# Performance work log

Hardware: AMD Instinct MI355X
Metric: run time of the kernel (lower is better)

Reference implementation:

```python
import jax, jax.numpy as jnp
import numpy as np

EMB, HID, NH = 512, 256, 8
DH = HID // NH
LN_EPS = 1e-5


def _mk(key, shape, scale=0.02):
    return jax.random.normal(key, shape, dtype=jnp.float32) * scale


def setup_inputs() -> dict:
    key = jax.random.key(0)
    ks = jax.random.split(key, 24)
    B, S = 8, 256
    return {
        "memory_embeddings": jax.random.normal(ks[0], (B, S, EMB), dtype=jnp.float32),
        # memory_encoder: Linear(512,256) -> LayerNorm -> ReLU -> Linear(256,256)
        "enc_w1": _mk(ks[1], (HID, EMB)), "enc_b1": jnp.zeros((HID,), jnp.float32),
        "ln_g": jnp.ones((HID,), jnp.float32), "ln_b": jnp.zeros((HID,), jnp.float32),
        "enc_w2": _mk(ks[2], (HID, HID)), "enc_b2": jnp.zeros((HID,), jnp.float32),
        # MultiheadAttention packed qkv + out proj
        "in_proj_w": _mk(ks[3], (3 * HID, HID)), "in_proj_b": jnp.zeros((3 * HID,), jnp.float32),
        "out_w": _mk(ks[4], (HID, HID)), "out_b": jnp.zeros((HID,), jnp.float32),
        # consistency head: Linear(256,128) -> ReLU -> Linear(128,1) -> Sigmoid
        "cons_w1": _mk(ks[5], (HID // 2, HID)), "cons_b1": jnp.zeros((HID // 2,), jnp.float32),
        "cons_w2": _mk(ks[6], (1, HID // 2)), "cons_b2": jnp.zeros((1,), jnp.float32),
        # hallucination detector
        "hall_w1": _mk(ks[7], (HID // 2, HID)), "hall_b1": jnp.zeros((HID // 2,), jnp.float32),
        "hall_w2": _mk(ks[8], (1, HID // 2)), "hall_b2": jnp.zeros((1,), jnp.float32),
        # contradiction analyzer: Linear(512,256) -> ReLU -> Linear(256,1) -> Sigmoid
        "con_w1": _mk(ks[9], (HID, 2 * HID)), "con_b1": jnp.zeros((HID,), jnp.float32),
        "con_w2": _mk(ks[10], (1, HID)), "con_b2": jnp.zeros((1,), jnp.float32),
    }


def _forward(memory_embeddings, enc_w1, enc_b1, ln_g, ln_b, enc_w2, enc_b2,
             in_proj_w, in_proj_b, out_w, out_b,
             cons_w1, cons_b1, cons_w2, cons_b2,
             hall_w1, hall_b1, hall_w2, hall_b2,
             con_w1, con_b1, con_w2, con_b2):
    B, S, _ = memory_embeddings.shape
    # --- memory encoder (dropout in eval mode = identity) ---
    h = memory_embeddings @ enc_w1.T + enc_b1                      # [B,S,HID]
    mu = h.mean(-1, keepdims=True)
    var = ((h - mu) ** 2).mean(-1, keepdims=True)
    h = (h - mu) * jax.lax.rsqrt(var + LN_EPS) * ln_g + ln_b
    mf = jax.nn.relu(h) @ enc_w2.T + enc_b2                        # [B,S,HID]
    # --- multihead self-attention (batch_first, averaged attn weights) ---
    qkv = mf @ in_proj_w.T + in_proj_b                              # [B,S,3H]
    q, k, v = jnp.split(qkv, 3, axis=-1)
    def heads(t):  # [B,S,H] -> [B,NH,S,DH]
        return t.reshape(B, S, NH, DH).transpose(0, 2, 1, 3)
    q, k, v = heads(q), heads(k), heads(v)
    scores = jnp.einsum('bhsd,bhtd->bhst', q, k) / jnp.sqrt(jnp.float32(DH))
    attn = jax.nn.softmax(scores, axis=-1)                          # [B,NH,S,S]
    ctx = jnp.einsum('bhst,bhtd->bhsd', attn, v)
    ctx = ctx.transpose(0, 2, 1, 3).reshape(B, S, HID)
    attended = ctx @ out_w.T + out_b                                # [B,S,HID]
    attn_weights = attn.mean(axis=1)                                # [B,S,S]
    # --- pooled heads ---
    pooled = attended.mean(axis=1)                                  # [B,HID]
    cons = jax.nn.sigmoid(jax.nn.relu(pooled @ cons_w1.T + cons_b1) @ cons_w2.T + cons_b2)[:, 0]
    hall = jax.nn.sigmoid(jax.nn.relu(pooled @ hall_w1.T + hall_b1) @ hall_w2.T + hall_b2)[:, 0]
    # --- contradiction matrix over all i<j pairs (vectorized gather/MLP/scatter) ---
    iu, ju = np.triu_indices(S, k=1)                                # static indices
    Wa, Wb = con_w1[:, :HID], con_w1[:, HID:]                       # split concat-linear
    a = mf @ Wa.T                                                   # [B,S,HID]
    b = mf @ Wb.T
    hid = jax.nn.relu(a[:, iu] + b[:, ju] + con_b1)                 # [B,P,HID]
    sc = jax.nn.sigmoid(hid @ con_w2.T + con_b2)[..., 0]            # [B,P]
    M = jnp.zeros((B, S, S), dtype=mf.dtype)
    M = M.at[:, iu, ju].set(sc)
    M = M.at[:, ju, iu].set(sc)
    return cons, hall, M, attn_weights


def reference(memory_embeddings, enc_w1, enc_b1, ln_g, ln_b, enc_w2, enc_b2,
              in_proj_w, in_proj_b, out_w, out_b,
              cons_w1, cons_b1, cons_w2, cons_b2,
              hall_w1, hall_b1, hall_w2, hall_b2,
              con_w1, con_b1, con_w2, con_b2):
    return _forward(memory_embeddings, enc_w1, enc_b1, ln_g, ln_b, enc_w2, enc_b2,
                    in_proj_w, in_proj_b, out_w, out_b,
                    cons_w1, cons_b1, cons_w2, cons_b2,
                    hall_w1, hall_b1, hall_w2, hall_b2,
                    con_w1, con_b1, con_w2, con_b2)
```

## Files before the change

### kernel.cpp

```cpp
#include <hip/hip_runtime.h>
#include <math.h>

typedef __attribute__((ext_vector_type(8))) short bf16x8;
typedef __attribute__((ext_vector_type(4))) float f32x4;

__device__ __forceinline__ short f2b(float f) {
  union { float f; unsigned u; } v; v.f = f;
  unsigned u = v.u + 0x7fffu + ((v.u >> 16) & 1u);
  return (short)(u >> 16);
}

__global__ __launch_bounds__(256) void k_cvt(
    const float* __restrict__ w1, const float* __restrict__ w2,
    const float* __restrict__ wq, const float* __restrict__ wc,
    unsigned short* __restrict__ o, float* __restrict__ poolctx) {
  if (blockIdx.x == 0) {
    float4 z = {0.f, 0.f, 0.f, 0.f};
    ((float4*)poolctx)[threadIdx.x] = z;
    ((float4*)poolctx)[threadIdx.x + 256] = z;
  }
  int base = (blockIdx.x * 256 + threadIdx.x) * 4;
#pragma unroll
  for (int u = 0; u < 4; ++u) {
    int idx = base + u;
    float v;
    if (idx < 131072) v = w1[idx];
    else if (idx < 196608) v = w2[idx - 131072];
    else if (idx < 393216) v = wq[idx - 196608];
    else {
      int i = idx - 393216, n = i >> 8, k = i & 255;
      v = (n < 256) ? wc[n * 512 + k] : wc[(n - 256) * 512 + 256 + k];
    }
    o[idx] = (unsigned short)f2b(v);
  }
}

__global__ __launch_bounds__(256) void k_enc(
    const float* __restrict__ me,
    const unsigned short* __restrict__ wb1, const float* __restrict__ b1,
    const float* __restrict__ g, const float* __restrict__ lb,
    const unsigned short* __restrict__ wb2, const float* __restrict__ b2,
    unsigned short* __restrict__ mfb) {
  __shared__ float hh[16 * 260];
  __shared__ unsigned short rA[16 * 264];
  __shared__ unsigned short mfs[16 * 256];
  int tid = threadIdx.x, lane = tid & 63, w = tid >> 6;
  int row0 = blockIdx.x * 16;
  int m = lane & 15, q = lane >> 4;

  {
    f32x4 acc[4];
#pragma unroll
    for (int i = 0; i < 4; ++i) acc[i] = (f32x4){0.f, 0.f, 0.f, 0.f};
    const float* ap = me + (size_t)(row0 + m) * 512 + q * 8;
    float4 pa0[4], pa1[4];
    bf16x8 pb[4][4];
#pragma unroll
    for (int d = 0; d < 4; ++d) {
      pa0[d] = *(const float4*)(ap + d * 32);
      pa1[d] = *(const float4*)(ap + d * 32 + 4);
#pragma unroll
      for (int nt = 0; nt < 4; ++nt)
        pb[d][nt] = *(const bf16x8*)(wb1 + (size_t)(w * 64 + nt * 16 + m) * 512 + d * 32 + q * 8);
    }
#pragma unroll
    for (int it = 0; it < 16; ++it) {
      int slot = it & 3;
      float4 a01 = pa0[slot], a23 = pa1[slot];
      bf16x8 bl0 = pb[slot][0], bl1 = pb[slot][1];
      bf16x8 bl2 = pb[slot][2], bl3 = pb[slot][3];
      if (it + 4 < 16) {
        pa0[slot] = *(const float4*)(ap + (it + 4) * 32);
        pa1[slot] = *(const float4*)(ap + (it + 4) * 32 + 4);
#pragma unroll
        for (int nt = 0; nt < 4; ++nt)
          pb[slot][nt] = *(const bf16x8*)(wb1 + (size_t)(w * 64 + nt * 16 + m) * 512 + (it + 4) * 32 + q * 8);
      }
      bf16x8 af;
      af[0] = f2b(a01.x); af[1] = f2b(a01.y); af[2] = f2b(a01.z); af[3] = f2b(a01.w);
      af[4] = f2b(a23.x); af[5] = f2b(a23.y); af[6] = f2b(a23.z); af[7] = f2b(a23.w);
      acc[0] = __builtin_amdgcn_mfma_f32_16x16x32_bf16(af, bl0, acc[0], 0, 0, 0);
      acc[1] = __builtin_amdgcn_mfma_f32_16x16x32_bf16(af, bl1, acc[1], 0, 0, 0);
      acc[2] = __builtin_amdgcn_mfma_f32_16x16x32_bf16(af, bl2, acc[2], 0, 0, 0);
      acc[3] = __builtin_amdgcn_mfma_f32_16x16x32_bf16(af, bl3, acc[3], 0, 0, 0);
    }
#pragma unroll
    for (int nt = 0; nt < 4; ++nt) {
      int col = w * 64 + nt * 16 + m;
      float bias = b1[col];
#pragma unroll
      for (int reg = 0; reg < 4; ++reg)
        hh[(q * 4 + reg) * 260 + col] = acc[nt][reg] + bias;
    }
  }
  __syncthreads();
  {
    float4 g4 = *(const float4*)(g + lane * 4);
    float4 lb4 = *(const float4*)(lb + lane * 4);
#pragma unroll
    for (int rr = 0; rr < 4; ++rr) {
      int r = w * 4 + rr;
      float4 v = *(const float4*)&hh[r * 260 + lane * 4];
      float s1 = v.x + v.y + v.z + v.w;
      float s2 = v.x * v.x + v.y * v.y + v.z * v.z + v.w * v.w;
#pragma unroll
      for (int o = 32; o > 0; o >>= 1) {
        s1 += __shfl_xor(s1, o, 64);
        s2 += __shfl_xor(s2, o, 64);
      }
      float mu = s1 * (1.f / 256.f);
      float var = s2 * (1.f / 256.f) - mu * mu;
      float rs = rsqrtf(var + 1e-5f);
      unsigned short y0 = (unsigned short)f2b(fmaxf((v.x - mu) * rs * g4.x + lb4.x, 0.f));
      unsigned short y1 = (unsigned short)f2b(fmaxf((v.y - mu) * rs * g4.y + lb4.y, 0.f));
      unsigned short y2 = (unsigned short)f2b(fmaxf((v.z - mu) * rs * g4.z + lb4.z, 0.f));
      unsigned short y3 = (unsigned short)f2b(fmaxf((v.w - mu) * rs * g4.w + lb4.w, 0.f));
      uint2 pk;
      pk.x = (unsigned)y0 | ((unsigned)y1 << 16);
      pk.y = (unsigned)y2 | ((unsigned)y3 << 16);
      *(uint2*)&rA[r * 264 + lane * 4] = pk;
    }
  }
  __syncthreads();
  {
    f32x4 acc[4];
#pragma unroll
    for (int i = 0; i < 4; ++i) acc[i] = (f32x4){0.f, 0.f, 0.f, 0.f};
    bf16x8 pb[4][4];
#pragma unroll
    for (int d = 0; d < 4; ++d)
#pragma unroll
      for (int nt = 0; nt < 4; ++nt)
        pb[d][nt] = *(const bf16x8*)(wb2 + (size_t)(w * 64 + nt * 16 + m) * 256 + d * 32 + q * 8);
#pragma unroll
    for (int it = 0; it < 8; ++it) {
      int slot = it & 3;
      bf16x8 bl0 = pb[slot][0], bl1 = pb[slot][1];
      bf16x8 bl2 = pb[slot][2], bl3 = pb[slot][3];
      if (it + 4 < 8) {
#pragma unroll
        for (int nt = 0; nt < 4; ++nt)
          pb[slot][nt] = *(const bf16x8*)(wb2 + (size_t)(w * 64 + nt * 16 + m) * 256 + (it + 4) * 32 + q * 8);
      }
      bf16x8 af = *(const bf16x8*)&rA[m * 264 + it * 32 + q * 8];
      acc[0] = __builtin_amdgcn_mfma_f32_16x16x32_bf16(af, bl0, acc[0], 0, 0, 0);
      acc[1] = __builtin_amdgcn_mfma_f32_16x16x32_bf16(af, bl1, acc[1], 0, 0, 0);
      acc[2] = __builtin_amdgcn_mfma_f32_16x16x32_bf16(af, bl2, acc[2], 0, 0, 0);
      acc[3] = __builtin_amdgcn_mfma_f32_16x16x32_bf16(af, bl3, acc[3], 0, 0, 0);
    }
#pragma unroll
    for (int nt = 0; nt < 4; ++nt) {
      int col = w * 64 + nt * 16 + m;
      float bias = b2[col];
#pragma unroll
      for (int reg = 0; reg < 4; ++reg)
        mfs[(q * 4 + reg) * 256 + col] = (unsigned short)f2b(acc[nt][reg] + bias);
    }
  }
  __syncthreads();
  {
    const uint4* src = (const uint4*)mfs;
    uint4* dst = (uint4*)(mfb + (size_t)row0 * 256);
    dst[tid] = src[tid];
    dst[tid + 256] = src[tid + 256];
  }
}

__global__ __launch_bounds__(256) void k_proj5(
    const unsigned short* __restrict__ mfb,
    const unsigned short* __restrict__ wqk,
    const unsigned short* __restrict__ wab,
    const float* __restrict__ bq, const float* __restrict__ cb1,
    float* __restrict__ qkv, float* __restrict__ amat,
    float* __restrict__ bmat) {
  int tid = threadIdx.x, lane = tid & 63, w = tid >> 6;
  int row0 = blockIdx.x * 16;
  int part = blockIdx.y;
  int m = lane & 15, q = lane >> 4;
  const unsigned short* W = (part < 3) ? (wqk + (size_t)part * 65536)
                                       : (wab + (size_t)(part - 3) * 65536);
  bf16x8 a[8];
#pragma unroll
  for (int ks = 0; ks < 8; ++ks)
    a[ks] = *(const bf16x8*)(mfb + (size_t)(row0 + m) * 256 + ks * 32 + q * 8);
  f32x4 acc[4];
#pragma unroll
  for (int i = 0; i < 4; ++i) acc[i] = (f32x4){0.f, 0.f, 0.f, 0.f};
  bf16x8 pb[4][4];
#pragma unroll
  for (int d = 0; d < 4; ++d)
#pragma unroll
    for (int nt = 0; nt < 4; ++nt)
      pb[d][nt] = *(const bf16x8*)(W + (size_t)(w * 64 + nt * 16 + m) * 256 + d * 32 + q * 8);
#pragma unroll
  for (int it = 0; it < 8; ++it) {
    int slot = it & 3;
    bf16x8 bl0 = pb[slot][0], bl1 = pb[slot][1];
    bf16x8 bl2 = pb[slot][2], bl3 = pb[slot][3];
    if (it + 4 < 8) {
#pragma unroll
      for (int nt = 0; nt < 4; ++nt)
        pb[slot][nt] = *(const bf16x8*)(W + (size_t)(w * 64 + nt * 16 + m) * 256 + (it + 4) * 32 + q * 8);
    }
    acc[0] = __builtin_amdgcn_mfma_f32_16x16x32_bf16(a[it], bl0, acc[0], 0, 0, 0);
    acc[1] = __builtin_amdgcn_mfma_f32_16x16x32_bf16(a[it], bl1, acc[1], 0, 0, 0);
    acc[2] = __builtin_amdgcn_mfma_f32_16x16x32_bf16(a[it], bl2, acc[2], 0, 0, 0);
    acc[3] = __builtin_amdgcn_mfma_f32_16x16x32_bf16(a[it], bl3, acc[3], 0, 0, 0);
  }
#pragma unroll
  for (int nt = 0; nt < 4; ++nt) {
    int col = w * 64 + nt * 16 + m;
    float bias;
    float* dst;
    int ld;
    if (part < 3) { bias = bq[part * 256 + col]; dst = qkv + part * 256; ld = 768; }
    else if (part == 3) { bias = cb1[col]; dst = amat; ld = 256; }
    else { bias = 0.f; dst = bmat; ld = 256; }
#pragma unroll
    for (int reg = 0; reg < 4; ++reg) {
      int row = row0 + q * 4 + reg;
      dst[(size_t)row * ld + col] = acc[nt][reg] + bias;
    }
  }
}

__global__ __launch_bounds__(256) void k_attn_fused(
    const float* __restrict__ qkv, unsigned short* __restrict__ attnb,
    float* __restrict__ poolctx) {
  __shared__ float qs[32 * 32];
  __shared__ unsigned short ps[32 * 264];
  __shared__ unsigned short vt[32 * 264];
  int blk = blockIdx.x;
  int sg = blk & 7, bh = blk >> 3, h = bh & 7, b = bh >> 3;
  int tid = threadIdx.x, lane = tid & 63, w = tid >> 6;
  {
    int r = tid >> 3, c4 = tid & 7;
    float4 v = *(const float4*)(qkv + ((size_t)(b * 256 + sg * 32 + r)) * 768 + h * 32 + c4 * 4);
    *(float4*)&qs[r * 32 + c4 * 4] = v;
  }
  {
    const float4* vr = (const float4*)(qkv + ((size_t)(b * 256 + tid)) * 768 + 512 + h * 32);
#pragma unroll
    for (int d4 = 0; d4 < 8; ++d4) {
      float4 vv = vr[d4];
      vt[(d4 * 4 + 0) * 264 + tid] = (unsigned short)f2b(vv.x);
      vt[(d4 * 4 + 1) * 264 + tid] = (unsigned short)f2b(vv.y);
      vt[(d4 * 4 + 2) * 264 + tid] = (unsigned short)f2b(vv.z);
      vt[(d4 * 4 + 3) * 264 + tid] = (unsigned short)f2b(vv.w);
    }
  }
  __syncthreads();
  int r0 = w * 8;
  float sc[8][4];
#pragma unroll
  for (int r = 0; r < 8; ++r)
#pragma unroll
    for (int tt = 0; tt < 4; ++tt) sc[r][tt] = 0.f;
#pragma unroll
  for (int tt = 0; tt < 4; ++tt) {
    int t = tt * 64 + lane;
    const float4* kp = (const float4*)(qkv + ((size_t)(b * 256 + t)) * 768 + 256 + h * 32);
#pragma unroll
    for (int d4 = 0; d4 < 8; ++d4) {
      float4 kv = kp[d4];
#pragma unroll
      for (int r = 0; r < 8; ++r) {
        float4 qv = *(const float4*)&qs[(r0 + r) * 32 + d4 * 4];
        sc[r][tt] += qv.x * kv.x + qv.y * kv.y + qv.z * kv.z + qv.w * kv.w;
      }
    }
  }
  const float scale = 0.17677669529663689f;
  for (int r = 0; r < 8; ++r) {
    float v0 = sc[r][0] * scale, v1 = sc[r][1] * scale;
    float v2 = sc[r][2] * scale, v3 = sc[r][3] * scale;
    float mx = fmaxf(fmaxf(v0, v1), fmaxf(v2, v3));
#pragma unroll
    for (int o = 32; o > 0; o >>= 1) mx = fmaxf(mx, __shfl_xor(mx, o, 64));
    float e0 = expf(v0 - mx), e1 = expf(v1 - mx), e2 = expf(v2 - mx), e3 = expf(v3 - mx);
    float s = e0 + e1 + e2 + e3;
#pragma unroll
    for (int o = 32; o > 0; o >>= 1) s += __shfl_xor(s, o, 64);
    float inv = 1.f / s;
    unsigned short* prow = ps + (r0 + r) * 264;
    prow[lane] = (unsigned short)f2b(e0 * inv);
    prow[64 + lane] = (unsigned short)f2b(e1 * inv);
    prow[128 + lane] = (unsigned short)f2b(e2 * inv);
    prow[192 + lane] = (unsigned short)f2b(e3 * inv);
  }
  __syncthreads();
  {
    int r = tid >> 3, seg = tid & 7;
    const uint4* src = (const uint4*)&ps[r * 264 + seg * 32];
    uint4* dst = (uint4*)(attnb + ((size_t)(bh * 256 + sg * 32 + r)) * 256 + seg * 32);
    dst[0] = src[0]; dst[1] = src[1]; dst[2] = src[2]; dst[3] = src[3];
  }
  {
    int mt = w & 1, dt = w >> 1;
    int mm = lane & 15, qq = lane >> 4;
    f32x4 a = (f32x4){0.f, 0.f, 0.f, 0.f};
#pragma unroll
    for (int ks = 0; ks < 256; ks += 32) {
      bf16x8 af = *(const bf16x8*)&ps[(mt * 16 + mm) * 264 + ks + qq * 8];
      bf16x8 bf = *(const bf16x8*)&vt[(dt * 16 + mm) * 264 + ks + qq * 8];
      a = __builtin_amdgcn_mfma_f32_16x16x32_bf16(af, bf, a, 0, 0, 0);
    }
    float colsum = a[0] + a[1] + a[2] + a[3];
    colsum += __shfl_xor(colsum, 16, 64);
    colsum += __shfl_xor(colsum, 32, 64);
    if (lane < 16)
      atomicAdd(&poolctx[b * 256 + h * 32 + dt * 16 + mm], colsum);
  }
}

__global__ __launch_bounds__(256) void k_attn_mean(
    const unsigned short* __restrict__ attnb, float* __restrict__ out_aw) {
  int gid = blockIdx.x * 256 + threadIdx.x;
  int b = gid >> 13, e8 = gid & 8191;
  size_t e = (size_t)e8 * 8;
  float s0 = 0, s1 = 0, s2 = 0, s3 = 0, s4 = 0, s5 = 0, s6 = 0, s7 = 0;
#pragma unroll
  for (int h = 0; h < 8; ++h) {
    uint4 v = *(const uint4*)(attnb + (((size_t)(b * 8 + h)) << 16) + e);
    s0 += __uint_as_float(v.x << 16); s1 += __uint_as_float(v.x & 0xffff0000u);
    s2 += __uint_as_float(v.y << 16); s3 += __uint_as_float(v.y & 0xffff0000u);
    s4 += __uint_as_float(v.z << 16); s5 += __uint_as_float(v.z & 0xffff0000u);
    s6 += __uint_as_float(v.w << 16); s7 += __uint_as_float(v.w & 0xffff0000u);
  }
  float* dst = out_aw + ((size_t)b << 16) + e;
  float4 r0 = {s0 * 0.125f, s1 * 0.125f, s2 * 0.125f, s3 * 0.125f};
  float4 r1 = {s4 * 0.125f, s5 * 0.125f, s6 * 0.125f, s7 * 0.125f};
  *(float4*)dst = r0;
  *(float4*)(dst + 4) = r1;
}

__global__ __launch_bounds__(256) void k_heads(
    const float* __restrict__ poolctx,
    const float* __restrict__ outw, const float* __restrict__ outb,
    const float* __restrict__ cw1, const float* __restrict__ cb1,
    const float* __restrict__ cw2, const float* __restrict__ cb2,
    const float* __restrict__ hw1, const float* __restrict__ hb1,
    const float* __restrict__ hw2, const float* __restrict__ hb2,
    float* __restrict__ out) {
  int b = blockIdx.x, j = threadIdx.x;
  __shared__ float pc[256];
  __shared__ float psh[256];
  __shared__ float red[4];
  pc[j] = poolctx[b * 256 + j] * (1.f / 256.f);
  __syncthreads();
  float s = outb[j];
  const float4* wr = (const float4*)(outw + (size_t)j * 256);
  for (int k4 = 0; k4 < 64; ++k4) {
    float4 wv = wr[k4];
    const float* p = pc + k4 * 4;
    s += p[0] * wv.x + p[1] * wv.y + p[2] * wv.z + p[3] * wv.w;
  }
  psh[j] = s;
  __syncthreads();
  int jj = j & 127;
  bool isH = j >= 128;
  const float* w1 = isH ? hw1 : cw1;
  const float* bb1 = isH ? hb1 : cb1;
  const float* w2 = isH ? hw2 : cw2;
  float a = bb1[jj];
  const float4* w1r = (const float4*)(w1 + (size_t)jj * 256);
  for (int k4 = 0; k4 < 64; ++k4) {
    float4 wv = w1r[k4];
    const float* p = psh + k4 * 4;
    a += p[0] * wv.x + p[1] * wv.y + p[2] * wv.z + p[3] * wv.w;
  }
  float v = fmaxf(a, 0.f) * w2[jj];
#pragma unroll
  for (int o = 32; o > 0; o >>= 1) v += __shfl_xor(v, o, 64);
  if ((j & 63) == 0) red[j >> 6] = v;
  __syncthreads();
  if (j == 0) {
    float c = red[0] + red[1] + cb2[0];
    float h = red[2] + red[3] + hb2[0];
    out[b] = 1.f / (1.f + expf(-c));
    out[8 + b] = 1.f / (1.f + expf(-h));
  }
}

__global__ __launch_bounds__(256) void k_pairs(
    const float* __restrict__ amat, const float* __restrict__ bmat,
    const float* __restrict__ cw2, const float* __restrict__ cb2,
    float* __restrict__ M) {
  __shared__ float As[32 * 130];
  __shared__ float Bs[32 * 130];
  __shared__ float w2s[256];
  int blk = blockIdx.x;
  int b = blk / 36, tix = blk % 36;
  int it = 0, rem = tix;
  while (rem >= 8 - it) { rem -= 8 - it; ++it; }
  int jt = it + rem;
  int tid = threadIdx.x;
  int tj = tid & 15, ti = tid >> 4;
  w2s[tid] = cw2[tid];
  float acc00 = 0, acc01 = 0, acc10 = 0, acc11 = 0;
  const float* Ab = amat + ((size_t)(b * 256 + it * 32)) * 256;
  const float* Bb = bmat + ((size_t)(b * 256 + jt * 32)) * 256;
  for (int ch = 0; ch < 2; ++ch) {
    __syncthreads();
#pragma unroll
    for (int k = 0; k < 4; ++k) {
      int f = tid + k * 256;
      int r = f >> 5, c4 = f & 31;
      float4 va = *(const float4*)(Ab + (size_t)r * 256 + ch * 128 + c4 * 4);
      float4 vb = *(const float4*)(Bb + (size_t)r * 256 + ch * 128 + c4 * 4);
      int la = r * 130 + c4 * 4;
      *(float2*)&As[la] = make_float2(va.x, va.y);
      *(float2*)&As[la + 2] = make_float2(va.z, va.w);
      *(float2*)&Bs[la] = make_float2(vb.x, vb.y);
      *(float2*)&Bs[la + 2] = make_float2(vb.z, vb.w);
    }
    __syncthreads();
    const float* a0 = As + (2 * ti) * 130;
    const float* a1 = a0 + 130;
    const float* b0 = Bs + (2 * tj) * 130;
    const float* b1 = b0 + 130;
    const float* w2c = w2s + ch * 128;
    for (int d = 0; d < 128; d += 4) {
#pragma unroll
      for (int k = 0; k < 4; ++k) {
        float w = w2c[d + k];
        float av0 = a0[d + k], av1 = a1[d + k];
        float bv0 = b0[d + k], bv1 = b1[d + k];
        acc00 += fmaxf(av0 + bv0, 0.f) * w;
        acc01 += fmaxf(av0 + bv1, 0.f) * w;
        acc10 += fmaxf(av1 + bv0, 0.f) * w;
        acc11 += fmaxf(av1 + bv1, 0.f) * w;
      }
    }
  }
  float c2 = cb2[0];
  float s00 = 1.f / (1.f + expf(-(acc00 + c2)));
  float s01 = 1.f / (1.f + expf(-(acc01 + c2)));
  float s10 = 1.f / (1.f + expf(-(acc10 + c2)));
  float s11 = 1.f / (1.f + expf(-(acc11 + c2)));
  float* Mb = M + ((size_t)b << 16);
  int i0 = it * 32 + 2 * ti, i1 = i0 + 1;
  int j0 = jt * 32 + 2 * tj, j1 = j0 + 1;
  if (it != jt) {
    Mb[i0 * 256 + j0] = s00; Mb[j0 * 256 + i0] = s00;
    Mb[i0 * 256 + j1] = s01; Mb[j1 * 256 + i0] = s01;
    Mb[i1 * 256 + j0] = s10; Mb[j0 * 256 + i1] = s10;
    Mb[i1 * 256 + j1] = s11; Mb[j1 * 256 + i1] = s11;
  } else {
    if (j0 > i0) { Mb[i0 * 256 + j0] = s00; Mb[j0 * 256 + i0] = s00; }
    else if (j0 == i0) Mb[i0 * 256 + j0] = 0.f;
    if (j1 > i0) { Mb[i0 * 256 + j1] = s01; Mb[j1 * 256 + i0] = s01; }
    if (j0 > i1) { Mb[i1 * 256 + j0] = s10; Mb[j0 * 256 + i1] = s10; }
    if (j1 > i1) { Mb[i1 * 256 + j1] = s11; Mb[j1 * 256 + i1] = s11; }
    else if (j1 == i1) Mb[i1 * 256 + j1] = 0.f;
  }
}

extern "C" void kernel_launch(void* const* d_in, const int* in_sizes, int n_in,
                              void* d_out, int out_size, void* d_ws, size_t ws_size,
                              hipStream_t stream) {
  const float* me        = (const float*)d_in[0];
  const float* enc_w1    = (const float*)d_in[1];
  const float* enc_b1    = (const float*)d_in[2];
  const float* ln_g      = (const float*)d_in[3];
  const float* ln_b      = (const float*)d_in[4];
  const float* enc_w2    = (const float*)d_in[5];
  const float* enc_b2    = (const float*)d_in[6];
  const float* in_proj_w = (const float*)d_in[7];
  const float* in_proj_b = (const float*)d_in[8];
  const float* out_w     = (const float*)d_in[9];
  const float* out_b     = (const float*)d_in[10];
  const float* cons_w1   = (const float*)d_in[11];
  const float* cons_b1   = (const float*)d_in[12];
  const float* cons_w2   = (const float*)d_in[13];
  const float* cons_b2   = (const float*)d_in[14];
  const float* hall_w1   = (const float*)d_in[15];
  const float* hall_b1   = (const float*)d_in[16];
  const float* hall_w2   = (const float*)d_in[17];
  const float* hall_b2   = (const float*)d_in[18];
  const float* con_w1    = (const float*)d_in[19];
  const float* con_b1    = (const float*)d_in[20];
  const float* con_w2    = (const float*)d_in[21];
  const float* con_b2    = (const float*)d_in[22];

  float* ws = (float*)d_ws;
  float* qkv  = ws;
  unsigned short* attnb = (unsigned short*)(ws + 1572864);
  float* amat = ws + 3670016;
  float* bmat = ws + 4194304;
  unsigned short* mfb = (unsigned short*)(ws + 4718592);
  unsigned short* wbf = (unsigned short*)(ws + 4980736);
  float* poolctx = ws + 5242880;

  unsigned short* wb1 = wbf;
  unsigned short* wb2 = wbf + 131072;
  unsigned short* wqk = wbf + 196608;
  unsigned short* wab = wbf + 393216;

  float* out    = (float*)d_out;
  float* out_M  = out + 16;
  float* out_aw = out + 16 + 524288;

  k_cvt<<<512, 256, 0, stream>>>(enc_w1, enc_w2, in_proj_w, con_w1, wbf, poolctx);
  k_enc<<<128, 256, 0, stream>>>(me, wb1, enc_b1, ln_g, ln_b, wb2, enc_b2, mfb);
  k_proj5<<<dim3(128, 5), 256, 0, stream>>>(mfb, wqk, wab, in_proj_b, con_b1,
                                            qkv, amat, bmat);
  k_attn_fused<<<512, 256, 0, stream>>>(qkv, attnb, poolctx);
  k_attn_mean<<<256, 256, 0, stream>>>(attnb, out_aw);
  k_heads<<<8, 256, 0, stream>>>(poolctx, out_w, out_b,
                                 cons_w1, cons_b1, cons_w2, cons_b2,
                                 hall_w1, hall_b1, hall_w2, hall_b2, out);
  k_pairs<<<288, 256, 0, stream>>>(amat, bmat, con_w2, con_b2, out_M);
}
```

Measured before the change: 201.8 us.

## Fold weight conversion into GEMMs and merge tail kernels into one launch

Removes the separate fp32-to-bf16 weight conversion kernel: the encoder and projection kernels now read fp32 weights and convert them in registers just before the MFMA. The encoder runs with 512 threads per block and 32 output columns per wave, and it also zeroes the pooled-context buffer. The attention-mean, heads and pair-scoring kernels are merged into one launch that dispatches on block index, and the pair kernel's shared tiles switch to float4 loads with a padded stride. This cuts two launches and a round trip of the converted weights through memory, at the cost of redundant conversion work in each block and more fp32 weight traffic.

```diff
diff --git a/kernel.cpp b/kernel.cpp
--- a/kernel.cpp
+++ b/kernel.cpp
@@ -10,87 +10,71 @@
   return (short)(u >> 16);
 }
 
-__global__ __launch_bounds__(256) void k_cvt(
-    const float* __restrict__ w1, const float* __restrict__ w2,
-    const float* __restrict__ wq, const float* __restrict__ wc,
-    unsigned short* __restrict__ o, float* __restrict__ poolctx) {
-  if (blockIdx.x == 0) {
-    float4 z = {0.f, 0.f, 0.f, 0.f};
-    ((float4*)poolctx)[threadIdx.x] = z;
-    ((float4*)poolctx)[threadIdx.x + 256] = z;
-  }
-  int base = (blockIdx.x * 256 + threadIdx.x) * 4;
-#pragma unroll
-  for (int u = 0; u < 4; ++u) {
-    int idx = base + u;
-    float v;
-    if (idx < 131072) v = w1[idx];
-    else if (idx < 196608) v = w2[idx - 131072];
-    else if (idx < 393216) v = wq[idx - 196608];
-    else {
-      int i = idx - 393216, n = i >> 8, k = i & 255;
-      v = (n < 256) ? wc[n * 512 + k] : wc[(n - 256) * 512 + 256 + k];
-    }
-    o[idx] = (unsigned short)f2b(v);
-  }
-}
-
-__global__ __launch_bounds__(256) void k_enc(
+__device__ __forceinline__ bf16x8 cvt8(float4 a, float4 b) {
+  bf16x8 r;
+  r[0] = f2b(a.x); r[1] = f2b(a.y); r[2] = f2b(a.z); r[3] = f2b(a.w);
+  r[4] = f2b(b.x); r[5] = f2b(b.y); r[6] = f2b(b.z); r[7] = f2b(b.w);
+  return r;
+}
+
+__global__ __launch_bounds__(512) void k_enc(
     const float* __restrict__ me,
-    const unsigned short* __restrict__ wb1, const float* __restrict__ b1,
+    const float* __restrict__ w1f, const float* __restrict__ b1,
     const float* __restrict__ g, const float* __restrict__ lb,
-    const unsigned short* __restrict__ wb2, const float* __restrict__ b2,
-    unsigned short* __restrict__ mfb) {
+    const float* __restrict__ w2f, const float* __restrict__ b2,
+    unsigned short* __restrict__ mfb, float* __restrict__ poolctx) {
   __shared__ float hh[16 * 260];
   __shared__ unsigned short rA[16 * 264];
   __shared__ unsigned short mfs[16 * 256];
   int tid = threadIdx.x, lane = tid & 63, w = tid >> 6;
   int row0 = blockIdx.x * 16;
   int m = lane & 15, q = lane >> 4;
-
-  {
-    f32x4 acc[4];
-#pragma unroll
-    for (int i = 0; i < 4; ++i) acc[i] = (f32x4){0.f, 0.f, 0.f, 0.f};
+  if (blockIdx.x == 0) {
+    float4 z = {0.f, 0.f, 0.f, 0.f};
+    ((float4*)poolctx)[tid] = z;
+  }
+  {
+    f32x4 acc0 = (f32x4){0.f, 0.f, 0.f, 0.f};
+    f32x4 acc1 = (f32x4){0.f, 0.f, 0.f, 0.f};
     const float* ap = me + (size_t)(row0 + m) * 512 + q * 8;
-    float4 pa0[4], pa1[4];
-    bf16x8 pb[4][4];
+    const float* bp0 = w1f + (size_t)(w * 32 + m) * 512 + q * 8;
+    const float* bp1 = w1f + (size_t)(w * 32 + 16 + m) * 512 + q * 8;
+    float4 pa[4][2], pb[4][2][2];
 #pragma unroll
     for (int d = 0; d < 4; ++d) {
-      pa0[d] = *(const float4*)(ap + d * 32);
-      pa1[d] = *(const float4*)(ap + d * 32 + 4);
-#pragma unroll
-      for (int nt = 0; nt < 4; ++nt)
-        pb[d][nt] = *(const bf16x8*)(wb1 + (size_t)(w * 64 + nt * 16 + m) * 512 + d * 32 + q * 8);
+      pa[d][0] = *(const float4*)(ap + d * 32);
+      pa[d][1] = *(const float4*)(ap + d * 32 + 4);
+      pb[d][0][0] = *(const float4*)(bp0 + d * 32);
+      pb[d][0][1] = *(const float4*)(bp0 + d * 32 + 4);
+      pb[d][1][0] = *(const float4*)(bp1 + d * 32);
+      pb[d][1][1] = *(const float4*)(bp1 + d * 32 + 4);
     }
 #pragma unroll
     for (int it = 0; it < 16; ++it) {
       int slot = it & 3;
-      float4 a01 = pa0[slot], a23 = pa1[slot];
-      bf16x8 bl0 = pb[slot][0], bl1 = pb[slot][1];
-      bf16x8 bl2 = pb[slot][2], bl3 = pb[slot][3];
+      float4 a0 = pa[slot][0], a1 = pa[slot][1];
+      float4 b00 = pb[slot][0][0], b01 = pb[slot][0][1];
+      float4 b10 = pb[slot][1][0], b11 = pb[slot][1][1];
       if (it + 4 < 16) {
-        pa0[slot] = *(const float4*)(ap + (it + 4) * 32);
-        pa1[slot] = *(const float4*)(ap + (it + 4) * 32 + 4);
-#pragma unroll
-        for (int nt = 0; nt < 4; ++nt)
-          pb[slot][nt] = *(const bf16x8*)(wb1 + (size_t)(w * 64 + nt * 16 + m) * 512 + (it + 4) * 32 + q * 8);
-      }
-      bf16x8 af;
-      af[0] = f2b(a01.x); af[1] = f2b(a01.y); af[2] = f2b(a01.z); af[3] = f2b(a01.w);
-      af[4] = f2b(a23.x); af[5] = f2b(a23.y); af[6] = f2b(a23.z); af[7] = f2b(a23.w);
-      acc[0] = __builtin_amdgcn_mfma_f32_16x16x32_bf16(af, bl0, acc[0], 0, 0, 0);
-      acc[1] = __builtin_amdgcn_mfma_f32_16x16x32_bf16(af, bl1, acc[1], 0, 0, 0);
-      acc[2] = __builtin_amdgcn_mfma_f32_16x16x32_bf16(af, bl2, acc[2], 0, 0, 0);
-      acc[3] = __builtin_amdgcn_mfma_f32_16x16x32_bf16(af, bl3, acc[3], 0, 0, 0);
-    }
-#pragma unroll
-    for (int nt = 0; nt < 4; ++nt) {
-      int col = w * 64 + nt * 16 + m;
+        pa[slot][0] = *(const float4*)(ap + (it + 4) * 32);
+        pa[slot][1] = *(const float4*)(ap + (it + 4) * 32 + 4);
+        pb[slot][0][0] = *(const float4*)(bp0 + (it + 4) * 32);
+        pb[slot][0][1] = *(const float4*)(bp0 + (it + 4) * 32 + 4);
+        pb[slot][1][0] = *(const float4*)(bp1 + (it + 4) * 32);
+        pb[slot][1][1] = *(const float4*)(bp1 + (it + 4) * 32 + 4);
+      }
+      bf16x8 af = cvt8(a0, a1);
+      acc0 = __builtin_amdgcn_mfma_f32_16x16x32_bf16(af, cvt8(b00, b01), acc0, 0, 0, 0);
+      acc1 = __builtin_amdgcn_mfma_f32_16x16x32_bf16(af, cvt8(b10, b11), acc1, 0, 0, 0);
+    }
+#pragma unroll
+    for (int nt = 0; nt < 2; ++nt) {
+      int col = w * 32 + nt * 16 + m;
       float bias = b1[col];
+      f32x4 a = nt ? acc1 : acc0;
 #pragma unroll
       for (int reg = 0; reg < 4; ++reg)
-        hh[(q * 4 + reg) * 260 + col] = acc[nt][reg] + bias;
+        hh[(q * 4 + reg) * 260 + col] = a[reg] + bias;
     }
   }
   __syncthreads();
@@ -98,8 +82,8 @@
     float4 g4 = *(const float4*)(g + lane * 4);
     float4 lb4 = *(const float4*)(lb + lane * 4);
 #pragma unroll
-    for (int rr = 0; rr < 4; ++rr) {
-      int r = w * 4 + rr;
+    for (int rr = 0; rr < 2; ++rr) {
+      int r = w * 2 + rr;
       float4 v = *(const float4*)&hh[r * 260 + lane * 4];
       float s1 = v.x + v.y + v.z + v.w;
       float s2 = v.x * v.x + v.y * v.y + v.z * v.z + v.w * v.w;
@@ -123,38 +107,41 @@
   }
   __syncthreads();
   {
-    f32x4 acc[4];
-#pragma unroll
-    for (int i = 0; i < 4; ++i) acc[i] = (f32x4){0.f, 0.f, 0.f, 0.f};
-    bf16x8 pb[4][4];
-#pragma unroll
-    for (int d = 0; d < 4; ++d)
-#pragma unroll
-      for (int nt = 0; nt < 4; ++nt)
-        pb[d][nt] = *(const bf16x8*)(wb2 + (size_t)(w * 64 + nt * 16 + m) * 256 + d * 32 + q * 8);
+    f32x4 acc0 = (f32x4){0.f, 0.f, 0.f, 0.f};
+    f32x4 acc1 = (f32x4){0.f, 0.f, 0.f, 0.f};
+    const float* cp0 = w2f + (size_t)(w * 32 + m) * 256 + q * 8;
+    const float* cp1 = w2f + (size_t)(w * 32 + 16 + m) * 256 + q * 8;
+    float4 pb[4][2][2];
+#pragma unroll
+    for (int d = 0; d < 4; ++d) {
+      pb[d][0][0] = *(const float4*)(cp0 + d * 32);
+      pb[d][0][1] = *(const float4*)(cp0 + d * 32 + 4);
+      pb[d][1][0] = *(const float4*)(cp1 + d * 32);
+      pb[d][1][1] = *(const float4*)(cp1 + d * 32 + 4);
+    }
 #pragma unroll
     for (int it = 0; it < 8; ++it) {
       int slot = it & 3;
-      bf16x8 bl0 = pb[slot][0], bl1 = pb[slot][1];
-      bf16x8 bl2 = pb[slot][2], bl3 = pb[slot][3];
+      float4 b00 = pb[slot][0][0], b01 = pb[slot][0][1];
+      float4 b10 = pb[slot][1][0], b11 = pb[slot][1][1];
       if (it + 4 < 8) {
-#pragma unroll
-        for (int nt = 0; nt < 4; ++nt)
-          pb[slot][nt] = *(const bf16x8*)(wb2 + (size_t)(w * 64 + nt * 16 + m) * 256 + (it + 4) * 32 + q * 8);
+        pb[slot][0][0] = *(const float4*)(cp0 + (it + 4) * 32);
+        pb[slot][0][1] = *(const float4*)(cp0 + (it + 4) * 32 + 4);
+        pb[slot][1][0] = *(const float4*)(cp1 + (it + 4) * 32);
+        pb[slot][1][1] = *(const float4*)(cp1 + (it + 4) * 32 + 4);
       }
       bf16x8 af = *(const bf16x8*)&rA[m * 264 + it * 32 + q * 8];
-      acc[0] = __builtin_amdgcn_mfma_f32_16x16x32_bf16(af, bl0, acc[0], 0, 0, 0);
-      acc[1] = __builtin_amdgcn_mfma_f32_16x16x32_bf16(af, bl1, acc[1], 0, 0, 0);
-      acc[2] = __builtin_amdgcn_mfma_f32_16x16x32_bf16(af, bl2, acc[2], 0, 0, 0);
-      acc[3] = __builtin_amdgcn_mfma_f32_16x16x32_bf16(af, bl3, acc[3], 0, 0, 0);
-    }
-#pragma unroll
-    for (int nt = 0; nt < 4; ++nt) {
-      int col = w * 64 + nt * 16 + m;
+      acc0 = __builtin_amdgcn_mfma_f32_16x16x32_bf16(af, cvt8(b00, b01), acc0, 0, 0, 0);
+      acc1 = __builtin_amdgcn_mfma_f32_16x16x32_bf16(af, cvt8(b10, b11), acc1, 0, 0, 0);
+    }
+#pragma unroll
+    for (int nt = 0; nt < 2; ++nt) {
+      int col = w * 32 + nt * 16 + m;
       float bias = b2[col];
+      f32x4 a = nt ? acc1 : acc0;
 #pragma unroll
       for (int reg = 0; reg < 4; ++reg)
-        mfs[(q * 4 + reg) * 256 + col] = (unsigned short)f2b(acc[nt][reg] + bias);
+        mfs[(q * 4 + reg) * 256 + col] = (unsigned short)f2b(a[reg] + bias);
     }
   }
   __syncthreads();
@@ -162,14 +149,12 @@
     const uint4* src = (const uint4*)mfs;
     uint4* dst = (uint4*)(mfb + (size_t)row0 * 256);
     dst[tid] = src[tid];
-    dst[tid + 256] = src[tid + 256];
   }
 }
 
 __global__ __launch_bounds__(256) void k_proj5(
     const unsigned short* __restrict__ mfb,
-    const unsigned short* __restrict__ wqk,
-    const unsigned short* __restrict__ wab,
+    const float* __restrict__ wq, const float* __restrict__ wc,
     const float* __restrict__ bq, const float* __restrict__ cb1,
     float* __restrict__ qkv, float* __restrict__ amat,
     float* __restrict__ bmat) {
@@ -177,8 +162,10 @@
   int row0 = blockIdx.x * 16;
   int part = blockIdx.y;
   int m = lane & 15, q = lane >> 4;
-  const unsigned short* W = (part < 3) ? (wqk + (size_t)part * 65536)
-                                       : (wab + (size_t)(part - 3) * 65536);
+  const float* Wbase;
+  size_t wstride;
+  if (part < 3) { Wbase = wq + (size_t)part * 256 * 256; wstride = 256; }
+  else { Wbase = wc + (part == 4 ? 256 : 0); wstride = 512; }
   bf16x8 a[8];
 #pragma unroll
   for (int ks = 0; ks < 8; ++ks)
@@ -186,26 +173,36 @@
   f32x4 acc[4];
 #pragma unroll
   for (int i = 0; i < 4; ++i) acc[i] = (f32x4){0.f, 0.f, 0.f, 0.f};
-  bf16x8 pb[4][4];
+  const float* bp[4];
+#pragma unroll
+  for (int nt = 0; nt < 4; ++nt)
+    bp[nt] = Wbase + (size_t)(w * 64 + nt * 16 + m) * wstride + q * 8;
+  float4 pb[4][4][2];
 #pragma unroll
   for (int d = 0; d < 4; ++d)
 #pragma unroll
-    for (int nt = 0; nt < 4; ++nt)
-      pb[d][nt] = *(const bf16x8*)(W + (size_t)(w * 64 + nt * 16 + m) * 256 + d * 32 + q * 8);
+    for (int nt = 0; nt < 4; ++nt) {
+      pb[d][nt][0] = *(const float4*)(bp[nt] + d * 32);
+      pb[d][nt][1] = *(const float4*)(bp[nt] + d * 32 + 4);
+    }
 #pragma unroll
   for (int it = 0; it < 8; ++it) {
     int slot = it & 3;
-    bf16x8 bl0 = pb[slot][0], bl1 = pb[slot][1];
-    bf16x8 bl2 = pb[slot][2], bl3 = pb[slot][3];
+    float4 b0l = pb[slot][0][0], b0h = pb[slot][0][1];
+    float4 b1l = pb[slot][1][0], b1h = pb[slot][1][1];
+    float4 b2l = pb[slot][2][0], b2h = pb[slot][2][1];
+    float4 b3l = pb[slot][3][0], b3h = pb[slot][3][1];
     if (it + 4 < 8) {
 #pragma unroll
-      for (int nt = 0; nt < 4; ++nt)
-        pb[slot][nt] = *(const bf16x8*)(W + (size_t)(w * 64 + nt * 16 + m) * 256 + (it + 4) * 32 + q * 8);
-    }
-    acc[0] = __builtin_amdgcn_mfma_f32_16x16x32_bf16(a[it], bl0, acc[0], 0, 0, 0);
-    acc[1] = __builtin_amdgcn_mfma_f32_16x16x32_bf16(a[it], bl1, acc[1], 0, 0, 0);
-    acc[2] = __builtin_amdgcn_mfma_f32_16x16x32_bf16(a[it], bl2, acc[2], 0, 0, 0);
-    acc[3] = __builtin_amdgcn_mfma_f32_16x16x32_bf16(a[it], bl3, acc[3], 0, 0, 0);
+      for (int nt = 0; nt < 4; ++nt) {
+        pb[slot][nt][0] = *(const float4*)(bp[nt] + (it + 4) * 32);
+        pb[slot][nt][1] = *(const float4*)(bp[nt] + (it + 4) * 32 + 4);
+      }
+    }
+    acc[0] = __builtin_amdgcn_mfma_f32_16x16x32_bf16(a[it], cvt8(b0l, b0h), acc[0], 0, 0, 0);
+    acc[1] = __builtin_amdgcn_mfma_f32_16x16x32_bf16(a[it], cvt8(b1l, b1h), acc[1], 0, 0, 0);
+    acc[2] = __builtin_amdgcn_mfma_f32_16x16x32_bf16(a[it], cvt8(b2l, b2h), acc[2], 0, 0, 0);
+    acc[3] = __builtin_amdgcn_mfma_f32_16x16x32_bf16(a[it], cvt8(b3l, b3h), acc[3], 0, 0, 0);
   }
 #pragma unroll
   for (int nt = 0; nt < 4; ++nt) {
@@ -313,146 +310,144 @@
   }
 }
 
-__global__ __launch_bounds__(256) void k_attn_mean(
-    const unsigned short* __restrict__ attnb, float* __restrict__ out_aw) {
-  int gid = blockIdx.x * 256 + threadIdx.x;
-  int b = gid >> 13, e8 = gid & 8191;
-  size_t e = (size_t)e8 * 8;
-  float s0 = 0, s1 = 0, s2 = 0, s3 = 0, s4 = 0, s5 = 0, s6 = 0, s7 = 0;
-#pragma unroll
-  for (int h = 0; h < 8; ++h) {
-    uint4 v = *(const uint4*)(attnb + (((size_t)(b * 8 + h)) << 16) + e);
-    s0 += __uint_as_float(v.x << 16); s1 += __uint_as_float(v.x & 0xffff0000u);
-    s2 += __uint_as_float(v.y << 16); s3 += __uint_as_float(v.y & 0xffff0000u);
-    s4 += __uint_as_float(v.z << 16); s5 += __uint_as_float(v.z & 0xffff0000u);
-    s6 += __uint_as_float(v.w << 16); s7 += __uint_as_float(v.w & 0xffff0000u);
-  }
-  float* dst = out_aw + ((size_t)b << 16) + e;
-  float4 r0 = {s0 * 0.125f, s1 * 0.125f, s2 * 0.125f, s3 * 0.125f};
-  float4 r1 = {s4 * 0.125f, s5 * 0.125f, s6 * 0.125f, s7 * 0.125f};
-  *(float4*)dst = r0;
-  *(float4*)(dst + 4) = r1;
-}
-
-__global__ __launch_bounds__(256) void k_heads(
+__global__ __launch_bounds__(256) void k_tail(
+    const float* __restrict__ amat, const float* __restrict__ bmat,
+    const float* __restrict__ conw2, const float* __restrict__ conb2,
+    float* __restrict__ M,
+    const unsigned short* __restrict__ attnb, float* __restrict__ out_aw,
     const float* __restrict__ poolctx,
     const float* __restrict__ outw, const float* __restrict__ outb,
-    const float* __restrict__ cw1, const float* __restrict__ cb1,
+    const float* __restrict__ cw1, const float* __restrict__ cb1h,
     const float* __restrict__ cw2, const float* __restrict__ cb2,
     const float* __restrict__ hw1, const float* __restrict__ hb1,
     const float* __restrict__ hw2, const float* __restrict__ hb2,
     float* __restrict__ out) {
-  int b = blockIdx.x, j = threadIdx.x;
-  __shared__ float pc[256];
-  __shared__ float psh[256];
-  __shared__ float red[4];
-  pc[j] = poolctx[b * 256 + j] * (1.f / 256.f);
-  __syncthreads();
-  float s = outb[j];
-  const float4* wr = (const float4*)(outw + (size_t)j * 256);
-  for (int k4 = 0; k4 < 64; ++k4) {
-    float4 wv = wr[k4];
-    const float* p = pc + k4 * 4;
-    s += p[0] * wv.x + p[1] * wv.y + p[2] * wv.z + p[3] * wv.w;
-  }
-  psh[j] = s;
-  __syncthreads();
-  int jj = j & 127;
-  bool isH = j >= 128;
-  const float* w1 = isH ? hw1 : cw1;
-  const float* bb1 = isH ? hb1 : cb1;
-  const float* w2 = isH ? hw2 : cw2;
-  float a = bb1[jj];
-  const float4* w1r = (const float4*)(w1 + (size_t)jj * 256);
-  for (int k4 = 0; k4 < 64; ++k4) {
-    float4 wv = w1r[k4];
-    const float* p = psh + k4 * 4;
-    a += p[0] * wv.x + p[1] * wv.y + p[2] * wv.z + p[3] * wv.w;
-  }
-  float v = fmaxf(a, 0.f) * w2[jj];
-#pragma unroll
-  for (int o = 32; o > 0; o >>= 1) v += __shfl_xor(v, o, 64);
-  if ((j & 63) == 0) red[j >> 6] = v;
-  __syncthreads();
-  if (j == 0) {
-    float c = red[0] + red[1] + cb2[0];
-    float h = red[2] + red[3] + hb2[0];
-    out[b] = 1.f / (1.f + expf(-c));
-    out[8 + b] = 1.f / (1.f + expf(-h));
-  }
-}
-
-__global__ __launch_bounds__(256) void k_pairs(
-    const float* __restrict__ amat, const float* __restrict__ bmat,
-    const float* __restrict__ cw2, const float* __restrict__ cb2,
-    float* __restrict__ M) {
-  __shared__ float As[32 * 130];
-  __shared__ float Bs[32 * 130];
-  __shared__ float w2s[256];
-  int blk = blockIdx.x;
-  int b = blk / 36, tix = blk % 36;
-  int it = 0, rem = tix;
-  while (rem >= 8 - it) { rem -= 8 - it; ++it; }
-  int jt = it + rem;
-  int tid = threadIdx.x;
-  int tj = tid & 15, ti = tid >> 4;
-  w2s[tid] = cw2[tid];
-  float acc00 = 0, acc01 = 0, acc10 = 0, acc11 = 0;
-  const float* Ab = amat + ((size_t)(b * 256 + it * 32)) * 256;
-  const float* Bb = bmat + ((size_t)(b * 256 + jt * 32)) * 256;
-  for (int ch = 0; ch < 2; ++ch) {
+  __shared__ float smem[32 * 132 * 2 + 256];
+  int bx = blockIdx.x, tid = threadIdx.x;
+  if (bx < 288) {
+    float* As = smem;
+    float* Bs = smem + 32 * 132;
+    float* w2s = smem + 32 * 132 * 2;
+    int b = bx / 36, tix = bx % 36;
+    int it = 0, rem = tix;
+    while (rem >= 8 - it) { rem -= 8 - it; ++it; }
+    int jt = it + rem;
+    int tj = tid & 15, ti = tid >> 4;
+    w2s[tid] = conw2[tid];
+    float acc00 = 0, acc01 = 0, acc10 = 0, acc11 = 0;
+    const float* Ab = amat + ((size_t)(b * 256 + it * 32)) * 256;
+    const float* Bb = bmat + ((size_t)(b * 256 + jt * 32)) * 256;
+    for (int ch = 0; ch < 2; ++ch) {
+      __syncthreads();
+#pragma unroll
+      for (int k = 0; k < 4; ++k) {
+        int f = tid + k * 256;
+        int r = f >> 5, c4 = f & 31;
+        float4 va = *(const float4*)(Ab + (size_t)r * 256 + ch * 128 + c4 * 4);
+        float4 vb = *(const float4*)(Bb + (size_t)r * 256 + ch * 128 + c4 * 4);
+        *(float4*)&As[r * 132 + c4 * 4] = va;
+        *(float4*)&Bs[r * 132 + c4 * 4] = vb;
+      }
+      __syncthreads();
+      const float* a0 = As + (2 * ti) * 132;
+      const float* a1 = a0 + 132;
+      const float* b0 = Bs + (2 * tj) * 132;
+      const float* b1 = b0 + 132;
+      const float* w2c = w2s + ch * 128;
+      for (int d = 0; d < 128; d += 4) {
+        float4 wv = *(const float4*)&w2c[d];
+        float4 av0 = *(const float4*)&a0[d];
+        float4 av1 = *(const float4*)&a1[d];
+        float4 bv0 = *(const float4*)&b0[d];
+        float4 bv1 = *(const float4*)&b1[d];
+        acc00 += fmaxf(av0.x + bv0.x, 0.f) * wv.x + fmaxf(av0.y + bv0.y, 0.f) * wv.y
+               + fmaxf(av0.z + bv0.z, 0.f) * wv.z + fmaxf(av0.w + bv0.w, 0.f) * wv.w;
+        acc01 += fmaxf(av0.x + bv1.x, 0.f) * wv.x + fmaxf(av0.y + bv1.y, 0.f) * wv.y
+               + fmaxf(av0.z + bv1.z, 0.f) * wv.z + fmaxf(av0.w + bv1.w, 0.f) * wv.w;
+        acc10 += fmaxf(av1.x + bv0.x, 0.f) * wv.x + fmaxf(av1.y + bv0.y, 0.f) * wv.y
+               + fmaxf(av1.z + bv0.z, 0.f) * wv.z + fmaxf(av1.w + bv0.w, 0.f) * wv.w;
+        acc11 += fmaxf(av1.x + bv1.x, 0.f) * wv.x + fmaxf(av1.y + bv1.y, 0.f) * wv.y
+               + fmaxf(av1.z + bv1.z, 0.f) * wv.z + fmaxf(av1.w + bv1.w, 0.f) * wv.w;
+      }
+    }
+    float c2 = conb2[0];
+    float s00 = 1.f / (1.f + expf(-(acc00 + c2)));
+    float s01 = 1.f / (1.f + expf(-(acc01 + c2)));
+    float s10 = 1.f / (1.f + expf(-(acc10 + c2)));
+    float s11 = 1.f / (1.f + expf(-(acc11 + c2)));
+    float* Mb = M + ((size_t)b << 16);
+    int i0 = it * 32 + 2 * ti, i1 = i0 + 1;
+    int j0 = jt * 32 + 2 * tj, j1 = j0 + 1;
+    if (it != jt) {
+      Mb[i0 * 256 + j0] = s00; Mb[j0 * 256 + i0] = s00;
+      Mb[i0 * 256 + j1] = s01; Mb[j1 * 256 + i0] = s01;
+      Mb[i1 * 256 + j0] = s10; Mb[j0 * 256 + i1] = s10;
+      Mb[i1 * 256 + j1] = s11; Mb[j1 * 256 + i1] = s11;
+    } else {
+      if (j0 > i0) { Mb[i0 * 256 + j0] = s00; Mb[j0 * 256 + i0] = s00; }
+      else if (j0 == i0) Mb[i0 * 256 + j0] = 0.f;
+      if (j1 > i0) { Mb[i0 * 256 + j1] = s01; Mb[j1 * 256 + i0] = s01; }
+      if (j0 > i1) { Mb[i1 * 256 + j0] = s10; Mb[j0 * 256 + i1] = s10; }
+      if (j1 > i1) { Mb[i1 * 256 + j1] = s11; Mb[j1 * 256 + i1] = s11; }
+      else if (j1 == i1) Mb[i1 * 256 + j1] = 0.f;
+    }
+  } else if (bx < 544) {
+    int gid = (bx - 288) * 256 + tid;
+    int b = gid >> 13, e8 = gid & 8191;
+    size_t e = (size_t)e8 * 8;
+    float s0 = 0, s1 = 0, s2 = 0, s3 = 0, s4 = 0, s5 = 0, s6 = 0, s7 = 0;
+#pragma unroll
+    for (int h = 0; h < 8; ++h) {
+      uint4 v = *(const uint4*)(attnb + (((size_t)(b * 8 + h)) << 16) + e);
+      s0 += __uint_as_float(v.x << 16); s1 += __uint_as_float(v.x & 0xffff0000u);
+      s2 += __uint_as_float(v.y << 16); s3 += __uint_as_float(v.y & 0xffff0000u);
+      s4 += __uint_as_float(v.z << 16); s5 += __uint_as_float(v.z & 0xffff0000u);
+      s6 += __uint_as_float(v.w << 16); s7 += __uint_as_float(v.w & 0xffff0000u);
+    }
+    float* dst = out_aw + ((size_t)b << 16) + e;
+    float4 r0 = {s0 * 0.125f, s1 * 0.125f, s2 * 0.125f, s3 * 0.125f};
+    float4 r1 = {s4 * 0.125f, s5 * 0.125f, s6 * 0.125f, s7 * 0.125f};
+    *(float4*)dst = r0;
+    *(float4*)(dst + 4) = r1;
+  } else {
+    float* pc = smem;
+    float* psh = smem + 256;
+    float* red = smem + 512;
+    int b = bx - 544, j = tid;
+    pc[j] = poolctx[b * 256 + j] * (1.f / 256.f);
     __syncthreads();
-#pragma unroll
-    for (int k = 0; k < 4; ++k) {
-      int f = tid + k * 256;
-      int r = f >> 5, c4 = f & 31;
-      float4 va = *(const float4*)(Ab + (size_t)r * 256 + ch * 128 + c4 * 4);
-      float4 vb = *(const float4*)(Bb + (size_t)r * 256 + ch * 128 + c4 * 4);
-      int la = r * 130 + c4 * 4;
-      *(float2*)&As[la] = make_float2(va.x, va.y);
-      *(float2*)&As[la + 2] = make_float2(va.z, va.w);
-      *(float2*)&Bs[la] = make_float2(vb.x, vb.y);
-      *(float2*)&Bs[la + 2] = make_float2(vb.z, vb.w);
-    }
+    float s = outb[j];
+    const float4* wr = (const float4*)(outw + (size_t)j * 256);
+    for (int k4 = 0; k4 < 64; ++k4) {
+      float4 wv = wr[k4];
+      const float* p = pc + k4 * 4;
+      s += p[0] * wv.x + p[1] * wv.y + p[2] * wv.z + p[3] * wv.w;
+    }
+    psh[j] = s;
     __syncthreads();
-    const float* a0 = As + (2 * ti) * 130;
-    const float* a1 = a0 + 130;
-    const float* b0 = Bs + (2 * tj) * 130;
-    const float* b1 = b0 + 130;
-    const float* w2c = w2s + ch * 128;
-    for (int d = 0; d < 128; d += 4) {
-#pragma unroll
-      for (int k = 0; k < 4; ++k) {
-        float w = w2c[d + k];
-        float av0 = a0[d + k], av1 = a1[d + k];
-        float bv0 = b0[d + k], bv1 = b1[d + k];
-        acc00 += fmaxf(av0 + bv0, 0.f) * w;
-        acc01 += fmaxf(av0 + bv1, 0.f) * w;
-        acc10 += fmaxf(av1 + bv0, 0.f) * w;
-        acc11 += fmaxf(av1 + bv1, 0.f) * w;
-      }
-    }
-  }
-  float c2 = cb2[0];
-  float s00 = 1.f / (1.f + expf(-(acc00 + c2)));
-  float s01 = 1.f / (1.f + expf(-(acc01 + c2)));
-  float s10 = 1.f / (1.f + expf(-(acc10 + c2)));
-  float s11 = 1.f / (1.f + expf(-(acc11 + c2)));
-  float* Mb = M + ((size_t)b << 16);
-  int i0 = it * 32 + 2 * ti, i1 = i0 + 1;
-  int j0 = jt * 32 + 2 * tj, j1 = j0 + 1;
-  if (it != jt) {
-    Mb[i0 * 256 + j0] = s00; Mb[j0 * 256 + i0] = s00;
-    Mb[i0 * 256 + j1] = s01; Mb[j1 * 256 + i0] = s01;
-    Mb[i1 * 256 + j0] = s10; Mb[j0 * 256 + i1] = s10;
-    Mb[i1 * 256 + j1] = s11; Mb[j1 * 256 + i1] = s11;
-  } else {
-    if (j0 > i0) { Mb[i0 * 256 + j0] = s00; Mb[j0 * 256 + i0] = s00; }
-    else if (j0 == i0) Mb[i0 * 256 + j0] = 0.f;
-    if (j1 > i0) { Mb[i0 * 256 + j1] = s01; Mb[j1 * 256 + i0] = s01; }
-    if (j0 > i1) { Mb[i1 * 256 + j0] = s10; Mb[j0 * 256 + i1] = s10; }
-    if (j1 > i1) { Mb[i1 * 256 + j1] = s11; Mb[j1 * 256 + i1] = s11; }
-    else if (j1 == i1) Mb[i1 * 256 + j1] = 0.f;
+    int jj = j & 127;
+    bool isH = j >= 128;
+    const float* w1 = isH ? hw1 : cw1;
+    const float* bb1 = isH ? hb1 : cb1h;
+    const float* w2 = isH ? hw2 : cw2;
+    float a = bb1[jj];
+    const float4* w1r = (const float4*)(w1 + (size_t)jj * 256);
+    for (int k4 = 0; k4 < 64; ++k4) {
+      float4 wv = w1r[k4];
+      const float* p = psh + k4 * 4;
+      a += p[0] * wv.x + p[1] * wv.y + p[2] * wv.z + p[3] * wv.w;
+    }
+    float v = fmaxf(a, 0.f) * w2[jj];
+#pragma unroll
+    for (int o = 32; o > 0; o >>= 1) v += __shfl_xor(v, o, 64);
+    if ((j & 63) == 0) red[j >> 6] = v;
+    __syncthreads();
+    if (j == 0) {
+      float c = red[0] + red[1] + cb2[0];
+      float h = red[2] + red[3] + hb2[0];
+      out[b] = 1.f / (1.f + expf(-c));
+      out[8 + b] = 1.f / (1.f + expf(-h));
+    }
   }
 }
 
@@ -489,26 +484,21 @@
   float* amat = ws + 3670016;
   float* bmat = ws + 4194304;
   unsigned short* mfb = (unsigned short*)(ws + 4718592);
-  unsigned short* wbf = (unsigned short*)(ws + 4980736);
-  float* poolctx = ws + 5242880;
-
-  unsigned short* wb1 = wbf;
-  unsigned short* wb2 = wbf + 131072;
-  unsigned short* wqk = wbf + 196608;
-  unsigned short* wab = wbf + 393216;
+  float* poolctx = ws + 4980736;
 
   float* out    = (float*)d_out;
   float* out_M  = out + 16;
   float* out_aw = out + 16 + 524288;
 
-  k_cvt<<<512, 256, 0, stream>>>(enc_w1, enc_w2, in_proj_w, con_w1, wbf, poolctx);
-  k_enc<<<128, 256, 0, stream>>>(me, wb1, enc_b1, ln_g, ln_b, wb2, enc_b2, mfb);
-  k_proj5<<<dim3(128, 5), 256, 0, stream>>>(mfb, wqk, wab, in_proj_b, con_b1,
+  k_enc<<<128, 512, 0, stream>>>(me, enc_w1, enc_b1, ln_g, ln_b,
+                                 enc_w2, enc_b2, mfb, poolctx);
+  k_proj5<<<dim3(128, 5), 256, 0, stream>>>(mfb, in_proj_w, con_w1,
+                                            in_proj_b, con_b1,
                                             qkv, amat, bmat);
   k_attn_fused<<<512, 256, 0, stream>>>(qkv, attnb, poolctx);
-  k_attn_mean<<<256, 256, 0, stream>>>(attnb, out_aw);
-  k_heads<<<8, 256, 0, stream>>>(poolctx, out_w, out_b,
-                                 cons_w1, cons_b1, cons_w2, cons_b2,
-                                 hall_w1, hall_b1, hall_w2, hall_b2, out);
-  k_pairs<<<288, 256, 0, stream>>>(amat, bmat, con_w2, con_b2, out_M);
-}
+  k_tail<<<552, 256, 0, stream>>>(amat, bmat, con_w2, con_b2, out_M,
+                                  attnb, out_aw, poolctx,
+                                  out_w, out_b,
+                                  cons_w1, cons_b1, cons_w2, cons_b2,
+                                  hall_w1, hall_b1, hall_w2, hall_b2, out);
+}
```

After: 211.2 us. +4.7%, slower.
